# Kernel tuning notes

Measured on AMD Instinct MI355X. Metric: run time of the kernel, lower is better.

## Reference

```python
import jax, jax.numpy as jnp
import numpy as np

B, D, C, OUT = 16384, 784, 2048, 10

def setup_inputs() -> dict:
    key = jax.random.key(0)
    k1, k2, k3 = jax.random.split(key, 3)
    x = jax.random.normal(k1, (B, D), dtype=jnp.float32)
    centres = jax.random.normal(k2, (C, D), dtype=jnp.float32)
    log_sigmas = jnp.zeros((C,), dtype=jnp.float32)
    W = jax.random.normal(k3, (OUT, C), dtype=jnp.float32) * (1.0 / np.sqrt(C))
    b = jnp.zeros((OUT,), dtype=jnp.float32)
    return {"x": x, "centres": centres, "log_sigmas": log_sigmas, "W": W, "b": b}

def reference(x, centres, log_sigmas, W, b):
    # (B, C, D) broadcast tensor the torch code materializes; same math).
    x2 = jnp.sum(x * x, axis=-1, keepdims=True)          # (B, 1)
    c2 = jnp.sum(centres * centres, axis=-1)             # (C,)
    d2 = jnp.maximum(x2 + c2[None, :] - 2.0 * (x @ centres.T), 0.0)  # (B, C)
    distances = jnp.sqrt(d2) / jnp.exp(log_sigmas)[None, :]          # (B, C)
    phi = jnp.exp(-(distances * distances))              # gaussian basis
    return phi @ W.T + b                                  # (B, OUT)
```

## Files before the change

kernel.cpp:

```cpp
#include <hip/hip_runtime.h>


#define B_ROWS 16384
#define D_DIM  784
#define C_DIM  2048
#define NOUT   10
#define NKC    26
#define NCG    128
#define LOG2E  1.4426950408889634f

typedef __attribute__((ext_vector_type(8))) __bf16 bf16x8;
typedef __attribute__((ext_vector_type(4))) float  f32x4;
typedef __attribute__((ext_vector_type(4))) unsigned short ushort4v;

__device__ __forceinline__ unsigned short f2bf(float f) {
  union { float f; unsigned int u; } v; v.f = f;
  unsigned int u = v.u;
  return (unsigned short)((u + 0x7fffu + ((u >> 16) & 1u)) >> 16);
}

template <int ROWS, int A_ORDER>
__global__ __launch_bounds__(256) void prep_pack(const float* __restrict__ src,
                                                 bf16x8* __restrict__ dst,
                                                 float* __restrict__ sq) {
  __shared__ unsigned short L[16 * 840];
  __shared__ float sqa[16];
  const int g = blockIdx.x;
  const int t = threadIdx.x;
  if (t < 16) sqa[t] = 0.f;
#pragma unroll
  for (int i = 0; i < 13; ++i) {
    const int chunk = t + 256 * i;
    const int row = chunk / 208;
    const int c4  = chunk % 208;
    const int k   = c4 * 4;
    ushort4v o = {0, 0, 0, 0};
    if (k + 4 <= D_DIM) {
      const float4 v = *(const float4*)(src + ((size_t)(g * 16 + row)) * D_DIM + k);
      o.x = f2bf(v.x); o.y = f2bf(v.y); o.z = f2bf(v.z); o.w = f2bf(v.w);
    }
    *(ushort4v*)&L[row * 840 + k] = o;
  }
  __syncthreads();
  const int w = t >> 6, lane = t & 63, q = lane >> 4, l16 = lane & 15;
  float part = 0.f;
  for (int i = 0; i < 7; ++i) {
    const int kc = w + 4 * i;
    if (kc < NKC) {
      union { bf16x8 v; __bf16 e[8]; } u;
      u.v = *(const bf16x8*)&L[l16 * 840 + kc * 32 + q * 8];
#pragma unroll
      for (int e = 0; e < 8; ++e) { const float x = (float)u.e[e]; part += x * x; }
      const size_t tile = A_ORDER ? ((size_t)g * NKC + kc)
                                  : ((size_t)kc * (ROWS / 16) + g);
      dst[tile * 64 + lane] = u.v;
    }
  }
  part += __shfl_down(part, 32);
  part += __shfl_down(part, 16);
  if (lane < 16) atomicAdd(&sqa[l16], part);
  __syncthreads();
  if (t < 16) sq[g * 16 + t] = sqa[t];
}

__global__ __launch_bounds__(256) void prep_misc(const float* __restrict__ ls,
                                                 const float* __restrict__ W,
                                                 const float* __restrict__ bias,
                                                 float* __restrict__ scale,
                                                 unsigned short* __restrict__ wb,
                                                 float* __restrict__ out) {
  const int i = blockIdx.x * 256 + threadIdx.x;
  if (i < B_ROWS * NOUT) out[i] = bias[i % NOUT];
  const int j = i - B_ROWS * NOUT;
  if (j >= 0 && j < 16 * C_DIM)
    wb[j] = ((j >> 11) < NOUT) ? f2bf(W[(j >> 11) * C_DIM + (j & 2047)]) : (unsigned short)0;
  const int k = j - 16 * C_DIM;
  if (k >= 0 && k < C_DIM) scale[k] = __expf(-2.f * ls[k]) * LOG2E;
}

__global__ __launch_bounds__(256, 4) void rbf_main(
    const bf16x8* __restrict__ apk, const bf16x8* __restrict__ cbp,
    const __bf16* __restrict__ wb,
    const float* __restrict__ x2, const float* __restrict__ c2,
    const float* __restrict__ scale, float* __restrict__ out) {
  __shared__ __bf16 Ph[64 * 264];
  __shared__ float x2s[64];

  const int tid  = threadIdx.x;
  const int w    = tid >> 6;
  const int lane = tid & 63;
  const int q    = lane >> 4;
  const int l16  = lane & 15;
  const int br   = blockIdx.x;
  const int bc   = blockIdx.y;
  const int brow = br * 64;
  const int bcol = bc * 256;

  if (tid < 64) x2s[tid] = x2[brow + tid];
  __syncthreads();

  const bf16x8* apA = apk + ((size_t)br * 4 * NKC) * 64 + lane;
  const bf16x8* cbw = cbp + ((size_t)(bc * 16 + w * 4)) * 64 + lane;

  f32x4 acc[4][4] = {};
  bf16x8 afc[4], bfc[4], afn[4], bfn[4];
#pragma unroll
  for (int i = 0; i < 4; ++i) afc[i] = apA[(size_t)i * NKC * 64];
#pragma unroll
  for (int j = 0; j < 4; ++j) bfc[j] = cbw[(size_t)j * 64];

#pragma unroll 2
  for (int kc = 0; kc < NKC; ++kc) {
    const int kn = (kc + 1 < NKC) ? kc + 1 : NKC - 1;
#pragma unroll
    for (int i = 0; i < 4; ++i) afn[i] = apA[((size_t)i * NKC + kn) * 64];
#pragma unroll
    for (int j = 0; j < 4; ++j) bfn[j] = cbw[((size_t)kn * NCG + j) * 64];
#pragma unroll
    for (int i = 0; i < 4; ++i)
#pragma unroll
      for (int j = 0; j < 4; ++j)
        acc[i][j] = __builtin_amdgcn_mfma_f32_16x16x32_bf16(afc[i], bfc[j], acc[i][j], 0, 0, 0);
#pragma unroll
    for (int i = 0; i < 4; ++i) afc[i] = afn[i];
#pragma unroll
    for (int j = 0; j < 4; ++j) bfc[j] = bfn[j];
  }

#pragma unroll
  for (int i = 0; i < 4; ++i) {
    float xv[4];
#pragma unroll
    for (int r = 0; r < 4; ++r) xv[r] = x2s[i * 16 + q * 4 + r];
#pragma unroll
    for (int j = 0; j < 4; ++j) {
      const int cl = w * 64 + j * 16 + l16;
      const float c2v = c2[bcol + cl];
      const float sc = scale[bcol + cl];
#pragma unroll
      for (int r = 0; r < 4; ++r) {
        const int rl = i * 16 + q * 4 + r;
        const float d2 = fmaxf(fmaf(-2.f, acc[i][j][r], xv[r] + c2v), 0.f);
        Ph[rl * 264 + cl] = (__bf16)__builtin_exp2f(-d2 * sc);
      }
    }
  }
  __syncthreads();

  f32x4 oacc = {};
#pragma unroll
  for (int kk = 0; kk < 8; ++kk) {
    const bf16x8 bw = *(const bf16x8*)&wb[(size_t)l16 * C_DIM + bcol + kk * 32 + q * 8];
    const bf16x8 ap = *(const bf16x8*)&Ph[(w * 16 + l16) * 264 + kk * 32 + q * 8];
    oacc = __builtin_amdgcn_mfma_f32_16x16x32_bf16(ap, bw, oacc, 0, 0, 0);
  }
  if (l16 < NOUT) {
#pragma unroll
    for (int r = 0; r < 4; ++r) {
      const int grow = brow + w * 16 + q * 4 + r;
      atomicAdd(&out[grow * NOUT + l16], oacc[r]);
    }
  }
}

extern "C" void kernel_launch(void* const* d_in, const int* in_sizes, int n_in,
                              void* d_out, int out_size, void* d_ws, size_t ws_size,
                              hipStream_t stream) {
  const float* x    = (const float*)d_in[0];
  const float* cen  = (const float*)d_in[1];
  const float* ls   = (const float*)d_in[2];
  const float* W    = (const float*)d_in[3];
  const float* bias = (const float*)d_in[4];
  float* out = (float*)d_out;

  unsigned char* ws = (unsigned char*)d_ws;
  bf16x8* apk = (bf16x8*)(ws);
  bf16x8* cbp = (bf16x8*)(ws + 27262976);
  unsigned short* wb = (unsigned short*)(ws + 30670848);
  float* x2 = (float*)(ws + 30736384);
  float* c2 = (float*)(ws + 30801920);
  float* sc = (float*)(ws + 30810112);

  prep_pack<B_ROWS, 1><<<B_ROWS / 16, 256, 0, stream>>>(x, apk, x2);
  prep_pack<C_DIM, 0><<<C_DIM / 16, 256, 0, stream>>>(cen, cbp, c2);
  prep_misc<<<(B_ROWS * NOUT + 16 * C_DIM + C_DIM + 255) / 256, 256, 0, stream>>>(
      ls, W, bias, sc, wb, out);
  rbf_main<<<dim3(256, 8), 256, 0, stream>>>(apk, cbp, (const __bf16*)wb, x2, c2, sc, out);
}
```

Baseline: 178.0 us.

## Enlarge rbf_main block tile to 128x256 with 64x128 per-wave tiles

Each block of the main kernel now covers 128 rows by 256 centres, and each wave computes a 64x128 sub-tile (4x8 MFMA accumulators) instead of 16x... per-wave 64x64. This doubles operand reuse per global fragment load and halves the grid. The cost is higher register pressure (launch bounds lowered to 2 blocks per SIMD group) and a larger LDS phi buffer. Two smaller changes ride along: the K-chunk count drops from 26 to 25, removing an all-zero padding chunk, and the phi row stride is padded to 272.

Measured after the change: 218.4 us. 22.7% more time.

```diff
diff --git a/kernel.cpp b/kernel.cpp
--- a/kernel.cpp
+++ b/kernel.cpp
@@ -5,9 +5,10 @@
 #define D_DIM  784
 #define C_DIM  2048
 #define NOUT   10
-#define NKC    26
+#define NKC    25
 #define NCG    128
 #define LOG2E  1.4426950408889634f
+#define PHLD   272
 
 typedef __attribute__((ext_vector_type(8))) __bf16 bf16x8;
 typedef __attribute__((ext_vector_type(4))) float  f32x4;
@@ -78,13 +79,13 @@
   if (k >= 0 && k < C_DIM) scale[k] = __expf(-2.f * ls[k]) * LOG2E;
 }
 
-__global__ __launch_bounds__(256, 4) void rbf_main(
+__global__ __launch_bounds__(256, 2) void rbf_main(
     const bf16x8* __restrict__ apk, const bf16x8* __restrict__ cbp,
     const __bf16* __restrict__ wb,
     const float* __restrict__ x2, const float* __restrict__ c2,
     const float* __restrict__ scale, float* __restrict__ out) {
-  __shared__ __bf16 Ph[64 * 264];
-  __shared__ float x2s[64];
+  __shared__ __bf16 Ph[128 * PHLD];
+  __shared__ float x2s[128];
 
   const int tid  = threadIdx.x;
   const int w    = tid >> 6;
@@ -93,21 +94,22 @@
   const int l16  = lane & 15;
   const int br   = blockIdx.x;
   const int bc   = blockIdx.y;
-  const int brow = br * 64;
+  const int brow = br * 128;
   const int bcol = bc * 256;
+  const int wr   = (w >> 1) * 64;
+  const int wc   = (w & 1) * 128;
 
-  if (tid < 64) x2s[tid] = x2[brow + tid];
-  __syncthreads();
+  if (tid < 128) x2s[tid] = x2[brow + tid];
 
-  const bf16x8* apA = apk + ((size_t)br * 4 * NKC) * 64 + lane;
-  const bf16x8* cbw = cbp + ((size_t)(bc * 16 + w * 4)) * 64 + lane;
+  const bf16x8* apA = apk + ((size_t)(br * 8 + (w >> 1) * 4) * NKC) * 64 + lane;
+  const bf16x8* cbw = cbp + ((size_t)(bc * 16 + (w & 1) * 8)) * 64 + lane;
 
-  f32x4 acc[4][4] = {};
-  bf16x8 afc[4], bfc[4], afn[4], bfn[4];
+  f32x4 acc[4][8] = {};
+  bf16x8 afc[4], bfc[8], afn[4], bfn[8];
 #pragma unroll
   for (int i = 0; i < 4; ++i) afc[i] = apA[(size_t)i * NKC * 64];
 #pragma unroll
-  for (int j = 0; j < 4; ++j) bfc[j] = cbw[(size_t)j * 64];
+  for (int j = 0; j < 8; ++j) bfc[j] = cbw[(size_t)j * 64];
 
 #pragma unroll 2
   for (int kc = 0; kc < NKC; ++kc) {
@@ -115,51 +117,57 @@
 #pragma unroll
     for (int i = 0; i < 4; ++i) afn[i] = apA[((size_t)i * NKC + kn) * 64];
 #pragma unroll
-    for (int j = 0; j < 4; ++j) bfn[j] = cbw[((size_t)kn * NCG + j) * 64];
+    for (int j = 0; j < 8; ++j) bfn[j] = cbw[((size_t)kn * NCG + j) * 64];
 #pragma unroll
     for (int i = 0; i < 4; ++i)
 #pragma unroll
-      for (int j = 0; j < 4; ++j)
+      for (int j = 0; j < 8; ++j)
         acc[i][j] = __builtin_amdgcn_mfma_f32_16x16x32_bf16(afc[i], bfc[j], acc[i][j], 0, 0, 0);
 #pragma unroll
     for (int i = 0; i < 4; ++i) afc[i] = afn[i];
 #pragma unroll
-    for (int j = 0; j < 4; ++j) bfc[j] = bfn[j];
+    for (int j = 0; j < 8; ++j) bfc[j] = bfn[j];
   }
+  __syncthreads();
 
 #pragma unroll
   for (int i = 0; i < 4; ++i) {
     float xv[4];
 #pragma unroll
-    for (int r = 0; r < 4; ++r) xv[r] = x2s[i * 16 + q * 4 + r];
+    for (int r = 0; r < 4; ++r) xv[r] = x2s[wr + i * 16 + q * 4 + r];
 #pragma unroll
-    for (int j = 0; j < 4; ++j) {
-      const int cl = w * 64 + j * 16 + l16;
+    for (int j = 0; j < 8; ++j) {
+      const int cl = wc + j * 16 + l16;
       const float c2v = c2[bcol + cl];
       const float sc = scale[bcol + cl];
 #pragma unroll
       for (int r = 0; r < 4; ++r) {
-        const int rl = i * 16 + q * 4 + r;
+        const int rl = wr + i * 16 + q * 4 + r;
         const float d2 = fmaxf(fmaf(-2.f, acc[i][j][r], xv[r] + c2v), 0.f);
-        Ph[rl * 264 + cl] = (__bf16)__builtin_exp2f(-d2 * sc);
+        Ph[rl * PHLD + cl] = (__bf16)__builtin_exp2f(-d2 * sc);
       }
     }
   }
   __syncthreads();
 
-  f32x4 oacc = {};
+  f32x4 oacc[2] = {};
 #pragma unroll
   for (int kk = 0; kk < 8; ++kk) {
     const bf16x8 bw = *(const bf16x8*)&wb[(size_t)l16 * C_DIM + bcol + kk * 32 + q * 8];
-    const bf16x8 ap = *(const bf16x8*)&Ph[(w * 16 + l16) * 264 + kk * 32 + q * 8];
-    oacc = __builtin_amdgcn_mfma_f32_16x16x32_bf16(ap, bw, oacc, 0, 0, 0);
+#pragma unroll
+    for (int mi = 0; mi < 2; ++mi) {
+      const bf16x8 ap = *(const bf16x8*)&Ph[(w * 32 + mi * 16 + l16) * PHLD + kk * 32 + q * 8];
+      oacc[mi] = __builtin_amdgcn_mfma_f32_16x16x32_bf16(ap, bw, oacc[mi], 0, 0, 0);
+    }
   }
   if (l16 < NOUT) {
 #pragma unroll
-    for (int r = 0; r < 4; ++r) {
-      const int grow = brow + w * 16 + q * 4 + r;
-      atomicAdd(&out[grow * NOUT + l16], oacc[r]);
-    }
+    for (int mi = 0; mi < 2; ++mi)
+#pragma unroll
+      for (int r = 0; r < 4; ++r) {
+        const int grow = brow + w * 32 + mi * 16 + q * 4 + r;
+        atomicAdd(&out[grow * NOUT + l16], oacc[mi][r]);
+      }
   }
 }
 
@@ -185,5 +193,5 @@
   prep_pack<C_DIM, 0><<<C_DIM / 16, 256, 0, stream>>>(cen, cbp, c2);
   prep_misc<<<(B_ROWS * NOUT + 16 * C_DIM + C_DIM + 255) / 256, 256, 0, stream>>>(
       ls, W, bias, sc, wb, out);
-  rbf_main<<<dim3(256, 8), 256, 0, stream>>>(apk, cbp, (const __bf16*)wb, x2, c2, sc, out);
+  rbf_main<<<dim3(128, 8), 256, 0, stream>>>(apk, cbp, (const __bf16*)wb, x2, c2, sc, out);
 }
```
